# Kernel optimization log

Measured on AMD Instinct MI355X. Metric: run time of the kernel, lower is better.

The kernel has to match this reference:

```python
import jax, jax.numpy as jnp
import numpy as np

TOP_K = 4

def _silu_and_mul(gu):
    g, u = jnp.split(gu, 2, axis=-1)
    return jax.nn.silu(g) * u

def setup_inputs() -> dict:
    key = jax.random.key(0)
    ks = jax.random.split(key, 7)
    H, E, I, Is = 2048, 16, 1408, 5632
    s = 0.02
    return {
        "hidden_states": jax.random.normal(ks[0], (4, 1024, H), dtype=jnp.float32),
        "gate_w": jax.random.normal(ks[1], (E, H), dtype=jnp.float32) * s,
        "sgate_w": jax.random.normal(ks[2], (1, H), dtype=jnp.float32) * s,
        "w13": jax.random.normal(ks[3], (E, 2 * I, H), dtype=jnp.float32) * s,
        "w2": jax.random.normal(ks[4], (E, H, I), dtype=jnp.float32) * s,
        "shared_gate_up_w": jax.random.normal(ks[5], (2 * Is, H), dtype=jnp.float32) * s,
        "shared_down_w": jax.random.normal(ks[6], (H, Is), dtype=jnp.float32) * s,
    }

def reference(hidden_states, gate_w, sgate_w, w13, w2, shared_gate_up_w, shared_down_w):
    B, S, H = hidden_states.shape
    x = hidden_states.reshape(-1, H)  # [M, H]
    E = gate_w.shape[0]

    # shared expert: SiluAndMul MLP gated by sigmoid(shared_expert_gate(x))
    shared = _silu_and_mul(x @ shared_gate_up_w.T) @ shared_down_w.T
    shared = shared * jax.nn.sigmoid(x @ sgate_w.T)  # [M, H]

    # router: softmax in fp32, top-k (NOT renormalized, per original code)
    router_logits = x @ gate_w.T
    routing_weights = jax.nn.softmax(router_logits.astype(jnp.float32), axis=-1)
    topk_w, topk_ids = jax.lax.top_k(routing_weights, TOP_K)  # [M, K]

    # loop over fixed expert set via scan; every token goes through each
    # expert, masked by its routing coefficient (0 if not routed)
    def body(acc, ew):
        w13_e, w2_e, e = ew
        coef = jnp.sum(jnp.where(topk_ids == e, topk_w, 0.0), axis=-1)  # [M]
        h = _silu_and_mul(x @ w13_e.T)  # [M, I]
        acc = acc + (h @ w2_e.T).astype(jnp.float32) * coef[:, None]
        return acc, None

    init = jnp.zeros((x.shape[0], H), dtype=jnp.float32)
    sparse_out, _ = jax.lax.scan(body, init, (w13, w2, jnp.arange(E)))
    out = shared + sparse_out.astype(x.dtype)
    return out.reshape(B, S, H)
```

## Files before the change

kernel.cpp:

```cpp
#include <hip/hip_runtime.h>
#include <hip/hip_bf16.h>

#define E_NUM 16
#define TOPK 4
#define H_DIM 2048
#define I_DIM 1408
#define IS_DIM 5632
#define M_TOK 4096

typedef __attribute__((ext_vector_type(8))) short short8;
typedef __attribute__((ext_vector_type(4))) float f32x4;

static __device__ __forceinline__ unsigned short f2bf(float f) {
    unsigned int u = __float_as_uint(f);
    unsigned int r = (u + 0x7FFFu + ((u >> 16) & 1u)) >> 16;
    return (unsigned short)r;
}

static __device__ __forceinline__ void gl16(const unsigned short* g, unsigned short* l) {
    __builtin_amdgcn_global_load_lds(
        (const __attribute__((address_space(1))) unsigned int*)g,
        (__attribute__((address_space(3))) unsigned int*)l, 16, 0, 0);
}

__global__ __launch_bounds__(256) void k_router(
    const float* __restrict__ x, const float* __restrict__ gw,
    const float* __restrict__ sgw, int* __restrict__ counts,
    int* __restrict__ ltok, float* __restrict__ lcoef, float* __restrict__ sg)
{
    const int wid = threadIdx.x >> 6, lane = threadIdx.x & 63;
    const int t = blockIdx.x * 4 + wid;
    const float* xr = x + (size_t)t * H_DIM;
    float xv[32];
#pragma unroll
    for (int i = 0; i < 32; ++i) xv[i] = xr[i * 64 + lane];

    float lg[E_NUM];
    for (int e = 0; e < E_NUM; ++e) {
        const float* g = gw + (size_t)e * H_DIM;
        float s = 0.f;
#pragma unroll
        for (int i = 0; i < 32; ++i) s += xv[i] * g[i * 64 + lane];
#pragma unroll
        for (int off = 32; off; off >>= 1) s += __shfl_xor(s, off);
        lg[e] = s;
    }
    {
        float s = 0.f;
#pragma unroll
        for (int i = 0; i < 32; ++i) s += xv[i] * sgw[i * 64 + lane];
#pragma unroll
        for (int off = 32; off; off >>= 1) s += __shfl_xor(s, off);
        if (lane == 0) sg[t] = 1.f / (1.f + __expf(-s));
    }
    float mx = lg[0];
#pragma unroll
    for (int e = 1; e < E_NUM; ++e) mx = fmaxf(mx, lg[e]);
    float sum = 0.f, w[E_NUM];
#pragma unroll
    for (int e = 0; e < E_NUM; ++e) { w[e] = __expf(lg[e] - mx); sum += w[e]; }
    float inv = 1.f / sum;
#pragma unroll
    for (int e = 0; e < E_NUM; ++e) w[e] *= inv;

    if (lane == 0) {
        for (int j = 0; j < TOPK; ++j) {
            float best = -1.f; int bi = 0;
            for (int e = 0; e < E_NUM; ++e) if (w[e] > best) { best = w[e]; bi = e; }
            int pos = atomicAdd(&counts[bi], 1);
            ltok[bi * M_TOK + pos]  = t;
            lcoef[bi * M_TOK + pos] = best;
            w[bi] = -2.f;
        }
    }
}

__global__ void k_prefix(const int* __restrict__ counts, int* __restrict__ base) {
    if (threadIdx.x == 0) {
        int a = 0;
        for (int e = 0; e < E_NUM; ++e) { base[e] = a; a += counts[e]; }
        base[E_NUM] = a;
    }
}

__global__ __launch_bounds__(256) void k_cvtw(const float* __restrict__ src,
                                              unsigned short* __restrict__ dst, size_t n8)
{
    size_t stride = (size_t)gridDim.x * 256;
    for (size_t t = (size_t)blockIdx.x * 256 + threadIdx.x; t < n8; t += stride) {
        size_t i = t * 8;
        float4 a = *(const float4*)(src + i);
        float4 b = *(const float4*)(src + i + 4);
        union { unsigned short u[8]; short8 v; } o;
        o.u[0] = f2bf(a.x); o.u[1] = f2bf(a.y); o.u[2] = f2bf(a.z); o.u[3] = f2bf(a.w);
        o.u[4] = f2bf(b.x); o.u[5] = f2bf(b.y); o.u[6] = f2bf(b.z); o.u[7] = f2bf(b.w);
        *(short8*)(dst + i) = o.v;
    }
}

template<int TWOI, int NOFF>
__global__ __launch_bounds__(256) void k_cvtp(const float* __restrict__ src,
                                              unsigned short* __restrict__ dst, size_t n8)
{
    size_t stride = (size_t)gridDim.x * 256;
    for (size_t t = (size_t)blockIdx.x * 256 + threadIdx.x; t < n8; t += stride) {
        size_t i = t * 8;
        unsigned drow = (unsigned)(i >> 11);
        unsigned col  = (unsigned)(i & 2047u);
        unsigned grp = drow / (unsigned)TWOI;
        unsigned rr  = drow - grp * (unsigned)TWOI;
        unsigned q = rr >> 4, rm = rr & 15u;
        unsigned srow = ((q >> 1) << 4) + rm + ((q & 1u) ? (unsigned)NOFF : 0u);
        const float* s = src + (((size_t)grp * TWOI + srow) << 11) + col;
        float4 a = *(const float4*)s;
        float4 b = *(const float4*)(s + 4);
        union { unsigned short u[8]; short8 v; } o;
        o.u[0] = f2bf(a.x); o.u[1] = f2bf(a.y); o.u[2] = f2bf(a.z); o.u[3] = f2bf(a.w);
        o.u[4] = f2bf(b.x); o.u[5] = f2bf(b.y); o.u[6] = f2bf(b.z); o.u[7] = f2bf(b.w);
        *(short8*)(dst + i) = o.v;
    }
}

template<int MODE, int KDIM, long long BSTR, int KSPLIT>
__global__ __launch_bounds__(512, 2) void k_gemm(
    const unsigned short* __restrict__ Abase,
    const unsigned short* __restrict__ Bbase,
    void* __restrict__ outp,
    const int* __restrict__ ltok, const float* __restrict__ lcoef,
    const int* __restrict__ counts, const int* __restrict__ basearr,
    const float* __restrict__ sg)
{
    constexpr bool UP = (MODE == 0 || MODE == 2);
    constexpr int OSTR = (MODE == 0) ? IS_DIM : I_DIM;
    constexpr int KCH = KDIM / KSPLIT;
    constexpr int NT = KCH / 64;

    extern __shared__ unsigned short smem[];
    unsigned short* sA = smem;
    unsigned short* sB = smem + 49152;

    const int tid = threadIdx.x;
    const int lane = tid & 63, wid = tid >> 6;
    const int wr = wid >> 1, wc = wid & 1;
    const int lr = lane & 15, lk = lane >> 4;

    const unsigned gx = gridDim.x, gy = gridDim.y;
    const unsigned nwg = gx * gy;
    const unsigned orig = blockIdx.y * gx + blockIdx.x;
    const unsigned q8 = nwg >> 3, r8 = nwg & 7;
    const unsigned xcd = orig & 7, off8 = orig >> 3;
    const unsigned wg = ((xcd < r8) ? xcd * (q8 + 1) : r8 * (q8 + 1) + (xcd - r8) * q8) + off8;
    const int n0 = (int)(wg / gy) * 128;
    const int r0 = (int)(wg % gy) * 256;
    const int e  = blockIdx.z;

    int cnt = M_TOK, gbase = 0;
    if constexpr (MODE == 2 || MODE == 3) {
        cnt = counts[e];
        if (r0 >= cnt) return;
        gbase = basearr[e];
    }
    const int kbeg = (KSPLIT > 1) ? e * KCH : 0;
    const unsigned short* Bexp = Bbase + (size_t)e * (size_t)BSTR;

    const unsigned short* aptr[2][2];
#pragma unroll
    for (int h = 0; h < 2; ++h) {
#pragma unroll
        for (int i = 0; i < 2; ++i) {
            const int eo = (i * 512 + tid) * 8;
            const int prow = eo >> 6;
            const int kch = ((eo >> 3) & 7) ^ (prow & 7);
            const int lrow = h * 128 + prow;
            int ar;
            if constexpr (MODE == 0 || MODE == 1) ar = r0 + lrow;
            else {
                int rr2 = r0 + lrow; if (rr2 > cnt - 1) rr2 = cnt - 1;
                ar = (MODE == 2) ? ltok[e * M_TOK + rr2] : (gbase + rr2);
            }
            aptr[h][i] = Abase + (size_t)ar * KDIM + kbeg + kch * 8;
        }
    }
    const unsigned short* bptr[2];
#pragma unroll
    for (int i = 0; i < 2; ++i) {
        const int eo = (i * 512 + tid) * 8;
        const int prow = eo >> 6;
        const int kch = ((eo >> 3) & 7) ^ (prow & 7);
        bptr[i] = Bexp + (size_t)(n0 + prow) * KDIM + kbeg + kch * 8;
    }

    f32x4 acc[4][4];
    const f32x4 z = {0.f, 0.f, 0.f, 0.f};
#pragma unroll
    for (int m = 0; m < 4; ++m)
#pragma unroll
        for (int n = 0; n < 4; ++n) acc[m][n] = z;

    auto STAGE = [&](int buf, int kt) {
#pragma unroll
        for (int i = 0; i < 2; ++i)
            gl16(aptr[0][i] + kt, &sA[buf * 16384 + (i * 512 + tid) * 8]);
#pragma unroll
        for (int i = 0; i < 2; ++i)
            gl16(aptr[1][i] + kt, &sA[buf * 16384 + 8192 + (i * 512 + tid) * 8]);
#pragma unroll
        for (int i = 0; i < 2; ++i)
            gl16(bptr[i] + kt, &sB[buf * 8192 + (i * 512 + tid) * 8]);
    };

    STAGE(0, 0);
    STAGE(1, 64);
    asm volatile("s_waitcnt vmcnt(6)" ::: "memory");
    __builtin_amdgcn_s_barrier();

    short8 af[8], bf[8];
    int rb = 0;

#pragma unroll 1
    for (int t = 0; t < NT; ++t) {
        const bool pf = (t + 2 < NT);
        int wb = rb + 2; if (wb >= 3) wb -= 3;
        const int cbA = rb * 16384, cbB = rb * 8192;

#pragma unroll
        for (int m = 0; m < 4; ++m) {
            const int row = wr * 64 + m * 16 + lr;
#pragma unroll
            for (int kk = 0; kk < 2; ++kk)
                af[m * 2 + kk] = *(const short8*)&sA[cbA + (row << 6) + ((((kk << 2) + lk) ^ (row & 7)) << 3)];
        }
#pragma unroll
        for (int n = 0; n < 4; ++n) {
            const int row = wc * 64 + n * 16 + lr;
#pragma unroll
            for (int kk = 0; kk < 2; ++kk)
                bf[n * 2 + kk] = *(const short8*)&sB[cbB + (row << 6) + ((((kk << 2) + lk) ^ (row & 7)) << 3)];
        }

        if (pf) STAGE(wb, (t + 2) * 64);

        __builtin_amdgcn_s_setprio(1);
#pragma unroll
        for (int kk = 0; kk < 2; ++kk)
#pragma unroll
            for (int n = 0; n < 4; ++n)
#pragma unroll
                for (int m = 0; m < 4; ++m)
                    acc[m][n] = __builtin_amdgcn_mfma_f32_16x16x32_bf16(af[m * 2 + kk], bf[n * 2 + kk], acc[m][n], 0, 0, 0);
        __builtin_amdgcn_s_setprio(0);

        if (pf) asm volatile("s_waitcnt vmcnt(6)" ::: "memory");
        else    asm volatile("s_waitcnt vmcnt(0)" ::: "memory");
        __builtin_amdgcn_s_barrier();

        rb = (rb + 1 == 3) ? 0 : rb + 1;
    }

    if constexpr (UP) {
        const int hc0 = (n0 >> 1) + wc * 32 + lr;
        unsigned short* hb = (unsigned short*)outp;
#pragma unroll
        for (int m = 0; m < 4; ++m) {
#pragma unroll
            for (int j = 0; j < 4; ++j) {
                const int r = wr * 64 + m * 16 + lk * 4 + j;
                bool ok; size_t orow;
                if constexpr (MODE == 0) { ok = true; orow = (size_t)(r0 + r) * OSTR; }
                else { ok = (r0 + r < cnt); orow = (size_t)(gbase + r0 + r) * OSTR; }
                if (ok) {
                    float g0 = acc[m][0][j], u0 = acc[m][1][j];
                    float g1 = acc[m][2][j], u1 = acc[m][3][j];
                    hb[orow + hc0]      = f2bf(g0 / (1.f + __expf(-g0)) * u0);
                    hb[orow + hc0 + 16] = f2bf(g1 / (1.f + __expf(-g1)) * u1);
                }
            }
        }
    } else {
        float* op = (float*)outp;
#pragma unroll
        for (int m = 0; m < 4; ++m) {
#pragma unroll
            for (int j = 0; j < 4; ++j) {
                const int r = wr * 64 + m * 16 + lk * 4 + j;
                int tok; float scale; bool ok;
                if constexpr (MODE == 1) {
                    tok = r0 + r; scale = sg[tok]; ok = true;
                } else {
                    ok = (r0 + r < cnt);
                    int idx = ok ? (e * M_TOK + r0 + r) : (e * M_TOK);
                    tok = ltok[idx]; scale = lcoef[idx];
                }
                if (ok) {
                    size_t orow = (size_t)tok * H_DIM;
#pragma unroll
                    for (int n = 0; n < 4; ++n) {
                        const int col = n0 + wc * 64 + n * 16 + lr;
                        atomicAdd(op + orow + col, acc[m][n][j] * scale);
                    }
                }
            }
        }
    }
}

extern "C" void kernel_launch(void* const* d_in, const int* in_sizes, int n_in,
                              void* d_out, int out_size, void* d_ws, size_t ws_size,
                              hipStream_t stream) {
    const float* x    = (const float*)d_in[0];
    const float* gw   = (const float*)d_in[1];
    const float* sgw  = (const float*)d_in[2];
    const float* w13  = (const float*)d_in[3];
    const float* w2   = (const float*)d_in[4];
    const float* sguw = (const float*)d_in[5];
    const float* sdw  = (const float*)d_in[6];
    float* out = (float*)d_out;

    char* ws = (char*)d_ws;
    unsigned short* xb    = (unsigned short*)ws;
    unsigned short* hbuf  = (unsigned short*)(ws + 16777216);
    unsigned short* w13b  = (unsigned short*)(ws + 62914560);
    unsigned short* w2b   = (unsigned short*)(ws + 247463936);
    unsigned short* sguwb = (unsigned short*)(ws + 339738624);
    unsigned short* sdwb  = (unsigned short*)(ws + 385875968);
    size_t so = 408944640ULL;
    int*   ltok   = (int*)  (ws + so);
    float* lcoef  = (float*)(ws + so + 262144);
    int*   counts = (int*)  (ws + so + 524288);
    int*   basep  = (int*)  (ws + so + 524288 + 256);
    float* sg     = (float*)(ws + so + 524288 + 512);

    hipMemsetAsync(counts, 0, 64, stream);
    hipMemsetAsync(out, 0, (size_t)out_size * sizeof(float), stream);
    k_router<<<M_TOK / 4, 256, 0, stream>>>(x, gw, sgw, counts, ltok, lcoef, sg);
    k_prefix<<<1, 64, 0, stream>>>(counts, basep);
    k_cvtw<<<4096, 256, 0, stream>>>(x, xb, (size_t)M_TOK * H_DIM / 8);
    k_cvtp<2 * IS_DIM, IS_DIM><<<8192, 256, 0, stream>>>(sguw, sguwb, (size_t)2 * IS_DIM * H_DIM / 8);
    k_cvtw<<<8192, 256, 0, stream>>>(sdw,  sdwb,  (size_t)H_DIM * IS_DIM / 8);
    k_cvtp<2 * I_DIM, I_DIM><<<8192, 256, 0, stream>>>(w13, w13b, (size_t)E_NUM * 2 * I_DIM * H_DIM / 8);
    k_cvtw<<<8192, 256, 0, stream>>>(w2,   w2b,   (size_t)E_NUM * H_DIM * I_DIM / 8);

    static const int DYN = 147456;
    (void)hipFuncSetAttribute(reinterpret_cast<const void*>(&k_gemm<0, 2048, 0LL, 1>),
                              hipFuncAttributeMaxDynamicSharedMemorySize, DYN);
    (void)hipFuncSetAttribute(reinterpret_cast<const void*>(&k_gemm<1, 5632, 0LL, 2>),
                              hipFuncAttributeMaxDynamicSharedMemorySize, DYN);
    (void)hipFuncSetAttribute(reinterpret_cast<const void*>(&k_gemm<2, 2048, 5767168LL, 1>),
                              hipFuncAttributeMaxDynamicSharedMemorySize, DYN);
    (void)hipFuncSetAttribute(reinterpret_cast<const void*>(&k_gemm<3, 1408, 2883584LL, 1>),
                              hipFuncAttributeMaxDynamicSharedMemorySize, DYN);

    k_gemm<0, 2048, 0LL, 1>
        <<<dim3(2 * IS_DIM / 128, M_TOK / 256, 1), 512, DYN, stream>>>(
            xb, sguwb, hbuf, ltok, lcoef, counts, basep, sg);
    k_gemm<1, 5632, 0LL, 2>
        <<<dim3(H_DIM / 128, M_TOK / 256, 2), 512, DYN, stream>>>(
            hbuf, sdwb, out, ltok, lcoef, counts, basep, sg);
    k_gemm<2, 2048, 5767168LL, 1>
        <<<dim3(2 * I_DIM / 128, M_TOK / 256, E_NUM), 512, DYN, stream>>>(
            xb, w13b, hbuf, ltok, lcoef, counts, basep, sg);
    k_gemm<3, 1408, 2883584LL, 1>
        <<<dim3(H_DIM / 128, M_TOK / 256, E_NUM), 512, DYN, stream>>>(
            hbuf, w2b, out, ltok, lcoef, counts, basep, sg);
}
```

Measured before the change: 1.197 ms.

## Switch GEMM to 32x32x16 MFMA tiles with matching weight interleave

Replaces the 16x16x32 bf16 MFMA tiling with 32x32x16 instructions, using a 2x2 grid of 32x32 accumulators per wave. The gate/up weight interleave in the conversion kernel moves from 16-row to 32-row groups so the SiLU-and-mul epilogue still pairs gate and up columns from the same lane. The LDS fragment reads now happen after the prefetch issue rather than before it. The larger MFMA gives more work per instruction and fewer LDS fragment reads per FLOP. In exchange, the epilogue indexing changes and atomics are issued with a different per-lane pattern.

```diff
diff --git a/kernel.cpp b/kernel.cpp
--- a/kernel.cpp
+++ b/kernel.cpp
@@ -10,6 +10,7 @@
 
 typedef __attribute__((ext_vector_type(8))) short short8;
 typedef __attribute__((ext_vector_type(4))) float f32x4;
+typedef __attribute__((ext_vector_type(16))) float f32x16;
 
 static __device__ __forceinline__ unsigned short f2bf(float f) {
     unsigned int u = __float_as_uint(f);
@@ -109,8 +110,8 @@
         unsigned col  = (unsigned)(i & 2047u);
         unsigned grp = drow / (unsigned)TWOI;
         unsigned rr  = drow - grp * (unsigned)TWOI;
-        unsigned q = rr >> 4, rm = rr & 15u;
-        unsigned srow = ((q >> 1) << 4) + rm + ((q & 1u) ? (unsigned)NOFF : 0u);
+        unsigned q = rr >> 5, rm = rr & 31u;
+        unsigned srow = ((q >> 1) << 5) + rm + ((q & 1u) ? (unsigned)NOFF : 0u);
         const float* s = src + (((size_t)grp * TWOI + srow) << 11) + col;
         float4 a = *(const float4*)s;
         float4 b = *(const float4*)(s + 4);
@@ -142,7 +143,7 @@
     const int tid = threadIdx.x;
     const int lane = tid & 63, wid = tid >> 6;
     const int wr = wid >> 1, wc = wid & 1;
-    const int lr = lane & 15, lk = lane >> 4;
+    const int l31 = lane & 31, lh = lane >> 5;
 
     const unsigned gx = gridDim.x, gy = gridDim.y;
     const unsigned nwg = gx * gy;
@@ -190,12 +191,13 @@
         bptr[i] = Bexp + (size_t)(n0 + prow) * KDIM + kbeg + kch * 8;
     }
 
-    f32x4 acc[4][4];
-    const f32x4 z = {0.f, 0.f, 0.f, 0.f};
-#pragma unroll
-    for (int m = 0; m < 4; ++m)
-#pragma unroll
-        for (int n = 0; n < 4; ++n) acc[m][n] = z;
+    f32x16 acc[2][2];
+#pragma unroll
+    for (int m = 0; m < 2; ++m)
+#pragma unroll
+        for (int n = 0; n < 2; ++n)
+#pragma unroll
+            for (int r = 0; r < 16; ++r) acc[m][n][r] = 0.f;
 
     auto STAGE = [&](int buf, int kt) {
 #pragma unroll
@@ -223,31 +225,36 @@
         int wb = rb + 2; if (wb >= 3) wb -= 3;
         const int cbA = rb * 16384, cbB = rb * 8192;
 
-#pragma unroll
-        for (int m = 0; m < 4; ++m) {
-            const int row = wr * 64 + m * 16 + lr;
-#pragma unroll
-            for (int kk = 0; kk < 2; ++kk)
-                af[m * 2 + kk] = *(const short8*)&sA[cbA + (row << 6) + ((((kk << 2) + lk) ^ (row & 7)) << 3)];
-        }
-#pragma unroll
-        for (int n = 0; n < 4; ++n) {
-            const int row = wc * 64 + n * 16 + lr;
-#pragma unroll
-            for (int kk = 0; kk < 2; ++kk)
-                bf[n * 2 + kk] = *(const short8*)&sB[cbB + (row << 6) + ((((kk << 2) + lk) ^ (row & 7)) << 3)];
-        }
-
         if (pf) STAGE(wb, (t + 2) * 64);
 
+#pragma unroll
+        for (int mi = 0; mi < 2; ++mi) {
+            const int row = wr * 64 + mi * 32 + l31;
+#pragma unroll
+            for (int s = 0; s < 4; ++s) {
+                const int c8 = (s << 1) + lh;
+                af[mi * 4 + s] = *(const short8*)&sA[cbA + (row << 6) + ((c8 ^ (row & 7)) << 3)];
+            }
+        }
+#pragma unroll
+        for (int nf = 0; nf < 2; ++nf) {
+            const int row = wc * 64 + nf * 32 + l31;
+#pragma unroll
+            for (int s = 0; s < 4; ++s) {
+                const int c8 = (s << 1) + lh;
+                bf[nf * 4 + s] = *(const short8*)&sB[cbB + (row << 6) + ((c8 ^ (row & 7)) << 3)];
+            }
+        }
+
         __builtin_amdgcn_s_setprio(1);
 #pragma unroll
-        for (int kk = 0; kk < 2; ++kk)
-#pragma unroll
-            for (int n = 0; n < 4; ++n)
-#pragma unroll
-                for (int m = 0; m < 4; ++m)
-                    acc[m][n] = __builtin_amdgcn_mfma_f32_16x16x32_bf16(af[m * 2 + kk], bf[n * 2 + kk], acc[m][n], 0, 0, 0);
+        for (int s = 0; s < 4; ++s)
+#pragma unroll
+            for (int nf = 0; nf < 2; ++nf)
+#pragma unroll
+                for (int mi = 0; mi < 2; ++mi)
+                    acc[mi][nf] = __builtin_amdgcn_mfma_f32_32x32x16_bf16(
+                        af[mi * 4 + s], bf[nf * 4 + s], acc[mi][nf], 0, 0, 0);
         __builtin_amdgcn_s_setprio(0);
 
         if (pf) asm volatile("s_waitcnt vmcnt(6)" ::: "memory");
@@ -258,31 +265,30 @@
     }
 
     if constexpr (UP) {
-        const int hc0 = (n0 >> 1) + wc * 32 + lr;
+        const int hc0 = (n0 >> 1) + wc * 32 + l31;
         unsigned short* hb = (unsigned short*)outp;
 #pragma unroll
-        for (int m = 0; m < 4; ++m) {
-#pragma unroll
-            for (int j = 0; j < 4; ++j) {
-                const int r = wr * 64 + m * 16 + lk * 4 + j;
+        for (int mi = 0; mi < 2; ++mi) {
+#pragma unroll
+            for (int reg = 0; reg < 16; ++reg) {
+                const int r = wr * 64 + mi * 32 + (reg & 3) + 8 * (reg >> 2) + 4 * lh;
                 bool ok; size_t orow;
                 if constexpr (MODE == 0) { ok = true; orow = (size_t)(r0 + r) * OSTR; }
                 else { ok = (r0 + r < cnt); orow = (size_t)(gbase + r0 + r) * OSTR; }
                 if (ok) {
-                    float g0 = acc[m][0][j], u0 = acc[m][1][j];
-                    float g1 = acc[m][2][j], u1 = acc[m][3][j];
-                    hb[orow + hc0]      = f2bf(g0 / (1.f + __expf(-g0)) * u0);
-                    hb[orow + hc0 + 16] = f2bf(g1 / (1.f + __expf(-g1)) * u1);
+                    float g = acc[mi][0][reg], u = acc[mi][1][reg];
+                    hb[orow + hc0] = f2bf(g / (1.f + __expf(-g)) * u);
                 }
             }
         }
     } else {
         float* op = (float*)outp;
-#pragma unroll
-        for (int m = 0; m < 4; ++m) {
-#pragma unroll
-            for (int j = 0; j < 4; ++j) {
-                const int r = wr * 64 + m * 16 + lk * 4 + j;
+        const int col0 = n0 + wc * 64 + l31;
+#pragma unroll
+        for (int mi = 0; mi < 2; ++mi) {
+#pragma unroll
+            for (int reg = 0; reg < 16; ++reg) {
+                const int r = wr * 64 + mi * 32 + (reg & 3) + 8 * (reg >> 2) + 4 * lh;
                 int tok; float scale; bool ok;
                 if constexpr (MODE == 1) {
                     tok = r0 + r; scale = sg[tok]; ok = true;
@@ -293,11 +299,8 @@
                 }
                 if (ok) {
                     size_t orow = (size_t)tok * H_DIM;
-#pragma unroll
-                    for (int n = 0; n < 4; ++n) {
-                        const int col = n0 + wc * 64 + n * 16 + lr;
-                        atomicAdd(op + orow + col, acc[m][n][j] * scale);
-                    }
+                    atomicAdd(op + orow + col0,      acc[mi][0][reg] * scale);
+                    atomicAdd(op + orow + col0 + 32, acc[mi][1][reg] * scale);
                 }
             }
         }
```

Result: slower. 1.339 ms (+11.9%).

## Replace triple-buffered 256x128 GEMM tile with single-buffered 128x128 static-LDS tile

Applied to the files above, without the earlier changes.

Shrinks the GEMM workgroup from 512 threads with a 256x128 tile and a 3-stage global_load_lds ring to 256 threads with a 128x128 tile held in static shared memory. The K loop becomes load, syncthreads, compute, syncthreads, with no prefetch overlap and no s_setprio. LDS per block drops sharply and more blocks can be resident, but memory latency is no longer hidden by the pipeline and A/B reuse per tile is halved.

```diff
diff --git a/kernel.cpp b/kernel.cpp
--- a/kernel.cpp
+++ b/kernel.cpp
@@ -122,7 +122,7 @@
 }
 
 template<int MODE, int KDIM, long long BSTR, int KSPLIT>
-__global__ __launch_bounds__(512, 2) void k_gemm(
+__global__ __launch_bounds__(256) void k_gemm(
     const unsigned short* __restrict__ Abase,
     const unsigned short* __restrict__ Bbase,
     void* __restrict__ outp,
@@ -133,11 +133,9 @@
     constexpr bool UP = (MODE == 0 || MODE == 2);
     constexpr int OSTR = (MODE == 0) ? IS_DIM : I_DIM;
     constexpr int KCH = KDIM / KSPLIT;
-    constexpr int NT = KCH / 64;
-
-    extern __shared__ unsigned short smem[];
-    unsigned short* sA = smem;
-    unsigned short* sB = smem + 49152;
+
+    __shared__ unsigned short sA[128 * 64];
+    __shared__ unsigned short sB[128 * 64];
 
     const int tid = threadIdx.x;
     const int lane = tid & 63, wid = tid >> 6;
@@ -151,7 +149,7 @@
     const unsigned xcd = orig & 7, off8 = orig >> 3;
     const unsigned wg = ((xcd < r8) ? xcd * (q8 + 1) : r8 * (q8 + 1) + (xcd - r8) * q8) + off8;
     const int n0 = (int)(wg / gy) * 128;
-    const int r0 = (int)(wg % gy) * 256;
+    const int r0 = (int)(wg % gy) * 128;
     const int e  = blockIdx.z;
 
     int cnt = M_TOK, gbase = 0;
@@ -163,31 +161,20 @@
     const int kbeg = (KSPLIT > 1) ? e * KCH : 0;
     const unsigned short* Bexp = Bbase + (size_t)e * (size_t)BSTR;
 
-    const unsigned short* aptr[2][2];
-#pragma unroll
-    for (int h = 0; h < 2; ++h) {
-#pragma unroll
-        for (int i = 0; i < 2; ++i) {
-            const int eo = (i * 512 + tid) * 8;
-            const int prow = eo >> 6;
-            const int kch = ((eo >> 3) & 7) ^ (prow & 7);
-            const int lrow = h * 128 + prow;
-            int ar;
-            if constexpr (MODE == 0 || MODE == 1) ar = r0 + lrow;
-            else {
-                int rr2 = r0 + lrow; if (rr2 > cnt - 1) rr2 = cnt - 1;
-                ar = (MODE == 2) ? ltok[e * M_TOK + rr2] : (gbase + rr2);
-            }
-            aptr[h][i] = Abase + (size_t)ar * KDIM + kbeg + kch * 8;
-        }
-    }
-    const unsigned short* bptr[2];
-#pragma unroll
-    for (int i = 0; i < 2; ++i) {
-        const int eo = (i * 512 + tid) * 8;
-        const int prow = eo >> 6;
-        const int kch = ((eo >> 3) & 7) ^ (prow & 7);
-        bptr[i] = Bexp + (size_t)(n0 + prow) * KDIM + kbeg + kch * 8;
+    const unsigned short* aptr[4];
+    const unsigned short* bptr[4];
+#pragma unroll
+    for (int i = 0; i < 4; ++i) {
+        const int c = i * 256 + tid;
+        const int row = c >> 3, c8 = c & 7;
+        int ar;
+        if constexpr (MODE == 0 || MODE == 1) ar = r0 + row;
+        else {
+            int rr2 = r0 + row; if (rr2 > cnt - 1) rr2 = cnt - 1;
+            ar = (MODE == 2) ? ltok[e * M_TOK + rr2] : (gbase + rr2);
+        }
+        aptr[i] = Abase + (size_t)ar * KDIM + kbeg + ((c8 ^ (row & 7)) << 3);
+        bptr[i] = Bexp + (size_t)(n0 + row) * KDIM + kbeg + ((c8 ^ (row & 7)) << 3);
     }
 
     f32x4 acc[4][4];
@@ -197,64 +184,34 @@
 #pragma unroll
         for (int n = 0; n < 4; ++n) acc[m][n] = z;
 
-    auto STAGE = [&](int buf, int kt) {
-#pragma unroll
-        for (int i = 0; i < 2; ++i)
-            gl16(aptr[0][i] + kt, &sA[buf * 16384 + (i * 512 + tid) * 8]);
-#pragma unroll
-        for (int i = 0; i < 2; ++i)
-            gl16(aptr[1][i] + kt, &sA[buf * 16384 + 8192 + (i * 512 + tid) * 8]);
-#pragma unroll
-        for (int i = 0; i < 2; ++i)
-            gl16(bptr[i] + kt, &sB[buf * 8192 + (i * 512 + tid) * 8]);
-    };
-
-    STAGE(0, 0);
-    STAGE(1, 64);
-    asm volatile("s_waitcnt vmcnt(6)" ::: "memory");
-    __builtin_amdgcn_s_barrier();
-
-    short8 af[8], bf[8];
-    int rb = 0;
-
 #pragma unroll 1
-    for (int t = 0; t < NT; ++t) {
-        const bool pf = (t + 2 < NT);
-        int wb = rb + 2; if (wb >= 3) wb -= 3;
-        const int cbA = rb * 16384, cbB = rb * 8192;
-
-#pragma unroll
-        for (int m = 0; m < 4; ++m) {
-            const int row = wr * 64 + m * 16 + lr;
-#pragma unroll
-            for (int kk = 0; kk < 2; ++kk)
-                af[m * 2 + kk] = *(const short8*)&sA[cbA + (row << 6) + ((((kk << 2) + lk) ^ (row & 7)) << 3)];
-        }
-#pragma unroll
-        for (int n = 0; n < 4; ++n) {
-            const int row = wc * 64 + n * 16 + lr;
-#pragma unroll
-            for (int kk = 0; kk < 2; ++kk)
-                bf[n * 2 + kk] = *(const short8*)&sB[cbB + (row << 6) + ((((kk << 2) + lk) ^ (row & 7)) << 3)];
-        }
-
-        if (pf) STAGE(wb, (t + 2) * 64);
-
-        __builtin_amdgcn_s_setprio(1);
-#pragma unroll
-        for (int kk = 0; kk < 2; ++kk)
+    for (int kt = 0; kt < KCH; kt += 64) {
+#pragma unroll
+        for (int i = 0; i < 4; ++i) gl16(aptr[i] + kt, &sA[(i * 256 + tid) << 3]);
+#pragma unroll
+        for (int i = 0; i < 4; ++i) gl16(bptr[i] + kt, &sB[(i * 256 + tid) << 3]);
+        __syncthreads();
+#pragma unroll
+        for (int kk = 0; kk < 2; ++kk) {
+            const int c8 = kk * 4 + lk;
+            short8 af[4], bf[4];
+#pragma unroll
+            for (int m = 0; m < 4; ++m) {
+                const int row = wr * 64 + m * 16 + lr;
+                af[m] = *(const short8*)&sA[(row << 6) + ((c8 ^ (row & 7)) << 3)];
+            }
+#pragma unroll
+            for (int n = 0; n < 4; ++n) {
+                const int row = wc * 64 + n * 16 + lr;
+                bf[n] = *(const short8*)&sB[(row << 6) + ((c8 ^ (row & 7)) << 3)];
+            }
 #pragma unroll
             for (int n = 0; n < 4; ++n)
 #pragma unroll
                 for (int m = 0; m < 4; ++m)
-                    acc[m][n] = __builtin_amdgcn_mfma_f32_16x16x32_bf16(af[m * 2 + kk], bf[n * 2 + kk], acc[m][n], 0, 0, 0);
-        __builtin_amdgcn_s_setprio(0);
-
-        if (pf) asm volatile("s_waitcnt vmcnt(6)" ::: "memory");
-        else    asm volatile("s_waitcnt vmcnt(0)" ::: "memory");
-        __builtin_amdgcn_s_barrier();
-
-        rb = (rb + 1 == 3) ? 0 : rb + 1;
+                    acc[m][n] = __builtin_amdgcn_mfma_f32_16x16x32_bf16(af[m], bf[n], acc[m][n], 0, 0, 0);
+        }
+        __syncthreads();
     }
 
     if constexpr (UP) {
@@ -340,26 +297,16 @@
     k_cvtp<2 * I_DIM, I_DIM><<<8192, 256, 0, stream>>>(w13, w13b, (size_t)E_NUM * 2 * I_DIM * H_DIM / 8);
     k_cvtw<<<8192, 256, 0, stream>>>(w2,   w2b,   (size_t)E_NUM * H_DIM * I_DIM / 8);
 
-    static const int DYN = 147456;
-    (void)hipFuncSetAttribute(reinterpret_cast<const void*>(&k_gemm<0, 2048, 0LL, 1>),
-                              hipFuncAttributeMaxDynamicSharedMemorySize, DYN);
-    (void)hipFuncSetAttribute(reinterpret_cast<const void*>(&k_gemm<1, 5632, 0LL, 2>),
-                              hipFuncAttributeMaxDynamicSharedMemorySize, DYN);
-    (void)hipFuncSetAttribute(reinterpret_cast<const void*>(&k_gemm<2, 2048, 5767168LL, 1>),
-                              hipFuncAttributeMaxDynamicSharedMemorySize, DYN);
-    (void)hipFuncSetAttribute(reinterpret_cast<const void*>(&k_gemm<3, 1408, 2883584LL, 1>),
-                              hipFuncAttributeMaxDynamicSharedMemorySize, DYN);
-
     k_gemm<0, 2048, 0LL, 1>
-        <<<dim3(2 * IS_DIM / 128, M_TOK / 256, 1), 512, DYN, stream>>>(
+        <<<dim3(2 * IS_DIM / 128, M_TOK / 128, 1), 256, 0, stream>>>(
             xb, sguwb, hbuf, ltok, lcoef, counts, basep, sg);
     k_gemm<1, 5632, 0LL, 2>
-        <<<dim3(H_DIM / 128, M_TOK / 256, 2), 512, DYN, stream>>>(
+        <<<dim3(H_DIM / 128, M_TOK / 128, 2), 256, 0, stream>>>(
             hbuf, sdwb, out, ltok, lcoef, counts, basep, sg);
     k_gemm<2, 2048, 5767168LL, 1>
-        <<<dim3(2 * I_DIM / 128, M_TOK / 256, E_NUM), 512, DYN, stream>>>(
+        <<<dim3(2 * I_DIM / 128, M_TOK / 128, E_NUM), 256, 0, stream>>>(
             xb, w13b, hbuf, ltok, lcoef, counts, basep, sg);
     k_gemm<3, 1408, 2883584LL, 1>
-        <<<dim3(H_DIM / 128, M_TOK / 256, E_NUM), 512, DYN, stream>>>(
+        <<<dim3(H_DIM / 128, M_TOK / 128, E_NUM), 256, 0, stream>>>(
             hbuf, w2b, out, ltok, lcoef, counts, basep, sg);
 }
```

Result: slower. 1.370 ms (+14.5%).

## Merge weight conversions into one kernel and fuse shared and expert down GEMMs

Applied to the files above, without the earlier changes.

Replaces the five separate fp32-to-bf16 conversion launches with one grid-stride kernel that dispatches on index range. The shared-expert down-projection and the routed-expert down-projection now run in a single launch, with the z dimension selecting which GEMM body to run. To make this possible, the expert up-projection writes its activations into the already-consumed shared gate/up weight buffer instead of hbuf. This cuts launch overhead and tail effects and lets the two down GEMMs fill the GPU together, at the cost of reusing a workspace buffer that must no longer be needed.

```diff
diff --git a/kernel.cpp b/kernel.cpp
--- a/kernel.cpp
+++ b/kernel.cpp
@@ -83,59 +83,65 @@
     }
 }
 
-__global__ __launch_bounds__(256) void k_cvtw(const float* __restrict__ src,
-                                              unsigned short* __restrict__ dst, size_t n8)
+__global__ __launch_bounds__(256) void k_cvtall(
+    const float* __restrict__ x, const float* __restrict__ sguw,
+    const float* __restrict__ sdw, const float* __restrict__ w13,
+    const float* __restrict__ w2,
+    unsigned short* __restrict__ xb, unsigned short* __restrict__ sguwb,
+    unsigned short* __restrict__ sdwb, unsigned short* __restrict__ w13b,
+    unsigned short* __restrict__ w2b)
 {
+    const size_t N0 = 1048576;
+    const size_t N1 = 3932160;
+    const size_t N2 = 5373952;
+    const size_t N3 = 16908288;
+    const size_t N4 = 22675456;
     size_t stride = (size_t)gridDim.x * 256;
-    for (size_t t = (size_t)blockIdx.x * 256 + threadIdx.x; t < n8; t += stride) {
-        size_t i = t * 8;
-        float4 a = *(const float4*)(src + i);
-        float4 b = *(const float4*)(src + i + 4);
-        union { unsigned short u[8]; short8 v; } o;
-        o.u[0] = f2bf(a.x); o.u[1] = f2bf(a.y); o.u[2] = f2bf(a.z); o.u[3] = f2bf(a.w);
-        o.u[4] = f2bf(b.x); o.u[5] = f2bf(b.y); o.u[6] = f2bf(b.z); o.u[7] = f2bf(b.w);
-        *(short8*)(dst + i) = o.v;
-    }
-}
-
-template<int TWOI, int NOFF>
-__global__ __launch_bounds__(256) void k_cvtp(const float* __restrict__ src,
-                                              unsigned short* __restrict__ dst, size_t n8)
-{
-    size_t stride = (size_t)gridDim.x * 256;
-    for (size_t t = (size_t)blockIdx.x * 256 + threadIdx.x; t < n8; t += stride) {
-        size_t i = t * 8;
-        unsigned drow = (unsigned)(i >> 11);
-        unsigned col  = (unsigned)(i & 2047u);
-        unsigned grp = drow / (unsigned)TWOI;
-        unsigned rr  = drow - grp * (unsigned)TWOI;
-        unsigned q = rr >> 4, rm = rr & 15u;
-        unsigned srow = ((q >> 1) << 4) + rm + ((q & 1u) ? (unsigned)NOFF : 0u);
-        const float* s = src + (((size_t)grp * TWOI + srow) << 11) + col;
+    for (size_t t = (size_t)blockIdx.x * 256 + threadIdx.x; t < N4; t += stride) {
+        const float* s; unsigned short* d;
+        if (t < N0) {
+            size_t i = t * 8; s = x + i; d = xb + i;
+        } else if (t < N1) {
+            size_t i = (t - N0) * 8;
+            unsigned drow = (unsigned)(i >> 11), col = (unsigned)(i & 2047u);
+            unsigned q = drow >> 4, rm = drow & 15u;
+            unsigned srow = ((q >> 1) << 4) + rm + ((q & 1u) ? (unsigned)IS_DIM : 0u);
+            s = sguw + ((size_t)srow << 11) + col; d = sguwb + i;
+        } else if (t < N2) {
+            size_t i = (t - N1) * 8; s = sdw + i; d = sdwb + i;
+        } else if (t < N3) {
+            size_t i = (t - N2) * 8;
+            unsigned drow = (unsigned)(i >> 11), col = (unsigned)(i & 2047u);
+            unsigned grp = drow / (2 * I_DIM), rr = drow - grp * (2 * I_DIM);
+            unsigned q = rr >> 4, rm = rr & 15u;
+            unsigned srow = ((q >> 1) << 4) + rm + ((q & 1u) ? (unsigned)I_DIM : 0u);
+            s = w13 + (((size_t)grp * (2 * I_DIM) + srow) << 11) + col; d = w13b + i;
+        } else {
+            size_t i = (t - N3) * 8; s = w2 + i; d = w2b + i;
+        }
         float4 a = *(const float4*)s;
         float4 b = *(const float4*)(s + 4);
         union { unsigned short u[8]; short8 v; } o;
         o.u[0] = f2bf(a.x); o.u[1] = f2bf(a.y); o.u[2] = f2bf(a.z); o.u[3] = f2bf(a.w);
         o.u[4] = f2bf(b.x); o.u[5] = f2bf(b.y); o.u[6] = f2bf(b.z); o.u[7] = f2bf(b.w);
-        *(short8*)(dst + i) = o.v;
-    }
-}
-
-template<int MODE, int KDIM, long long BSTR, int KSPLIT>
-__global__ __launch_bounds__(512, 2) void k_gemm(
+        *(short8*)d = o.v;
+    }
+}
+
+template<int MODE, int KDIM, int KCH, long long BSTR>
+__device__ __forceinline__ void gemm_body(
     const unsigned short* __restrict__ Abase,
     const unsigned short* __restrict__ Bbase,
     void* __restrict__ outp,
     const int* __restrict__ ltok, const float* __restrict__ lcoef,
     const int* __restrict__ counts, const int* __restrict__ basearr,
-    const float* __restrict__ sg)
+    const float* __restrict__ sg,
+    unsigned short* smem, const int n0, const int r0, const int e, const int kbeg)
 {
     constexpr bool UP = (MODE == 0 || MODE == 2);
     constexpr int OSTR = (MODE == 0) ? IS_DIM : I_DIM;
-    constexpr int KCH = KDIM / KSPLIT;
     constexpr int NT = KCH / 64;
 
-    extern __shared__ unsigned short smem[];
     unsigned short* sA = smem;
     unsigned short* sB = smem + 49152;
 
@@ -143,16 +149,6 @@
     const int lane = tid & 63, wid = tid >> 6;
     const int wr = wid >> 1, wc = wid & 1;
     const int lr = lane & 15, lk = lane >> 4;
-
-    const unsigned gx = gridDim.x, gy = gridDim.y;
-    const unsigned nwg = gx * gy;
-    const unsigned orig = blockIdx.y * gx + blockIdx.x;
-    const unsigned q8 = nwg >> 3, r8 = nwg & 7;
-    const unsigned xcd = orig & 7, off8 = orig >> 3;
-    const unsigned wg = ((xcd < r8) ? xcd * (q8 + 1) : r8 * (q8 + 1) + (xcd - r8) * q8) + off8;
-    const int n0 = (int)(wg / gy) * 128;
-    const int r0 = (int)(wg % gy) * 256;
-    const int e  = blockIdx.z;
 
     int cnt = M_TOK, gbase = 0;
     if constexpr (MODE == 2 || MODE == 3) {
@@ -160,7 +156,6 @@
         if (r0 >= cnt) return;
         gbase = basearr[e];
     }
-    const int kbeg = (KSPLIT > 1) ? e * KCH : 0;
     const unsigned short* Bexp = Bbase + (size_t)e * (size_t)BSTR;
 
     const unsigned short* aptr[2][2];
@@ -304,6 +299,56 @@
     }
 }
 
+static __device__ __forceinline__ void xcd_swz(int& n0, int& r0) {
+    const unsigned gx = gridDim.x, gy = gridDim.y;
+    const unsigned nwg = gx * gy;
+    const unsigned orig = blockIdx.y * gx + blockIdx.x;
+    const unsigned q8 = nwg >> 3, r8 = nwg & 7;
+    const unsigned xcd = orig & 7, off8 = orig >> 3;
+    const unsigned wg = ((xcd < r8) ? xcd * (q8 + 1) : r8 * (q8 + 1) + (xcd - r8) * q8) + off8;
+    n0 = (int)(wg / gy) * 128;
+    r0 = (int)(wg % gy) * 256;
+}
+
+template<int MODE, int KDIM, int KCH, long long BSTR>
+__global__ __launch_bounds__(512, 2) void k_gemm(
+    const unsigned short* __restrict__ Abase,
+    const unsigned short* __restrict__ Bbase,
+    void* __restrict__ outp,
+    const int* __restrict__ ltok, const float* __restrict__ lcoef,
+    const int* __restrict__ counts, const int* __restrict__ basearr,
+    const float* __restrict__ sg)
+{
+    extern __shared__ unsigned short smem[];
+    int n0, r0;
+    xcd_swz(n0, r0);
+    gemm_body<MODE, KDIM, KCH, BSTR>(Abase, Bbase, outp, ltok, lcoef, counts,
+                                     basearr, sg, smem, n0, r0, blockIdx.z, 0);
+}
+
+__global__ __launch_bounds__(512, 2) void k_down(
+    const unsigned short* __restrict__ hs,
+    const unsigned short* __restrict__ he,
+    const unsigned short* __restrict__ sdwb,
+    const unsigned short* __restrict__ w2b,
+    float* __restrict__ out,
+    const int* __restrict__ ltok, const float* __restrict__ lcoef,
+    const int* __restrict__ counts, const int* __restrict__ basearr,
+    const float* __restrict__ sg)
+{
+    extern __shared__ unsigned short smem[];
+    int n0, r0;
+    xcd_swz(n0, r0);
+    const int z = blockIdx.z;
+    if (z < 2) {
+        gemm_body<1, 5632, 2816, 0LL>(hs, sdwb, out, ltok, lcoef, counts,
+                                      basearr, sg, smem, n0, r0, 0, z * 2816);
+    } else {
+        gemm_body<3, 1408, 1408, 2883584LL>(he, w2b, out, ltok, lcoef, counts,
+                                            basearr, sg, smem, n0, r0, z - 2, 0);
+    }
+}
+
 extern "C" void kernel_launch(void* const* d_in, const int* in_sizes, int n_in,
                               void* d_out, int out_size, void* d_ws, size_t ws_size,
                               hipStream_t stream) {
@@ -323,6 +368,7 @@
     unsigned short* w2b   = (unsigned short*)(ws + 247463936);
     unsigned short* sguwb = (unsigned short*)(ws + 339738624);
     unsigned short* sdwb  = (unsigned short*)(ws + 385875968);
+    unsigned short* he    = sguwb;
     size_t so = 408944640ULL;
     int*   ltok   = (int*)  (ws + so);
     float* lcoef  = (float*)(ws + so + 262144);
@@ -334,32 +380,23 @@
     hipMemsetAsync(out, 0, (size_t)out_size * sizeof(float), stream);
     k_router<<<M_TOK / 4, 256, 0, stream>>>(x, gw, sgw, counts, ltok, lcoef, sg);
     k_prefix<<<1, 64, 0, stream>>>(counts, basep);
-    k_cvtw<<<4096, 256, 0, stream>>>(x, xb, (size_t)M_TOK * H_DIM / 8);
-    k_cvtp<2 * IS_DIM, IS_DIM><<<8192, 256, 0, stream>>>(sguw, sguwb, (size_t)2 * IS_DIM * H_DIM / 8);
-    k_cvtw<<<8192, 256, 0, stream>>>(sdw,  sdwb,  (size_t)H_DIM * IS_DIM / 8);
-    k_cvtp<2 * I_DIM, I_DIM><<<8192, 256, 0, stream>>>(w13, w13b, (size_t)E_NUM * 2 * I_DIM * H_DIM / 8);
-    k_cvtw<<<8192, 256, 0, stream>>>(w2,   w2b,   (size_t)E_NUM * H_DIM * I_DIM / 8);
+    k_cvtall<<<8192, 256, 0, stream>>>(x, sguw, sdw, w13, w2,
+                                       xb, sguwb, sdwb, w13b, w2b);
 
     static const int DYN = 147456;
-    (void)hipFuncSetAttribute(reinterpret_cast<const void*>(&k_gemm<0, 2048, 0LL, 1>),
+    (void)hipFuncSetAttribute(reinterpret_cast<const void*>(&k_gemm<0, 2048, 2048, 0LL>),
                               hipFuncAttributeMaxDynamicSharedMemorySize, DYN);
-    (void)hipFuncSetAttribute(reinterpret_cast<const void*>(&k_gemm<1, 5632, 0LL, 2>),
+    (void)hipFuncSetAttribute(reinterpret_cast<const void*>(&k_gemm<2, 2048, 2048, 5767168LL>),
                               hipFuncAttributeMaxDynamicSharedMemorySize, DYN);
-    (void)hipFuncSetAttribute(reinterpret_cast<const void*>(&k_gemm<2, 2048, 5767168LL, 1>),
+    (void)hipFuncSetAttribute(reinterpret_cast<const void*>(&k_down),
                               hipFuncAttributeMaxDynamicSharedMemorySize, DYN);
-    (void)hipFuncSetAttribute(reinterpret_cast<const void*>(&k_gemm<3, 1408, 2883584LL, 1>),
-                              hipFuncAttributeMaxDynamicSharedMemorySize, DYN);
-
-    k_gemm<0, 2048, 0LL, 1>
+
+    k_gemm<0, 2048, 2048, 0LL>
         <<<dim3(2 * IS_DIM / 128, M_TOK / 256, 1), 512, DYN, stream>>>(
             xb, sguwb, hbuf, ltok, lcoef, counts, basep, sg);
-    k_gemm<1, 5632, 0LL, 2>
-        <<<dim3(H_DIM / 128, M_TOK / 256, 2), 512, DYN, stream>>>(
-            hbuf, sdwb, out, ltok, lcoef, counts, basep, sg);
-    k_gemm<2, 2048, 5767168LL, 1>
+    k_gemm<2, 2048, 2048, 5767168LL>
         <<<dim3(2 * I_DIM / 128, M_TOK / 256, E_NUM), 512, DYN, stream>>>(
-            xb, w13b, hbuf, ltok, lcoef, counts, basep, sg);
-    k_gemm<3, 1408, 2883584LL, 1>
-        <<<dim3(H_DIM / 128, M_TOK / 256, E_NUM), 512, DYN, stream>>>(
-            hbuf, w2b, out, ltok, lcoef, counts, basep, sg);
-}
+            xb, w13b, he, ltok, lcoef, counts, basep, sg);
+    k_down<<<dim3(H_DIM / 128, M_TOK / 256, 2 + E_NUM), 512, DYN, stream>>>(
+        hbuf, he, sdwb, w2b, out, ltok, lcoef, counts, basep, sg);
+}
```

After: 1.196 ms. Within noise of the previous version (-0.1%).
